# Kernel tuning notes

Measured on AMD Instinct MI355X. Metric: run time of the kernel, lower is better.

Reference implementation:

```python
import jax, jax.numpy as jnp
import numpy as np

THETA = 10000.0
B, S, D, H = 2, 2048, 1024, 16
DK = D // H


def setup_inputs() -> dict:
    key = jax.random.key(0)
    k1, k2, k3 = jax.random.split(key, 3)
    x = jax.random.normal(k1, (B, S, D), jnp.float32)
    # trunc_normal init approximated by scaled normal (std = 2/(d_k+d_model))
    weight = jax.random.normal(k2, (3, H, DK, D), jnp.float32) * (2.0 / (DK + D))
    wo_weight = jax.random.normal(k3, (D, H * DK), jnp.float32) * (2.0 / (2 * D))
    token_positions = jnp.arange(S, dtype=jnp.int32)
    return {"x": x, "token_positions": token_positions, "weight": weight, "wo_weight": wo_weight}


def _rope(x, cos, sin):
    # x: (..., seq, d_k); rotate interleaved pairs
    x1 = jnp.stack((-x[..., 1::2], x[..., ::2]), axis=-1).reshape(x.shape)
    return x * cos + x1 * sin


def _masked_softmax(scores, mask):
    # matches reference: exp(x - rowmax over ALL entries), zero masked, normalize, zero again
    e = jnp.exp(scores - jnp.max(scores, axis=-1, keepdims=True))
    e = jnp.where(mask, e, 0.0)
    a = e / jnp.sum(e, axis=-1, keepdims=True)
    return jnp.where(mask, a, 0.0)


def reference(x, token_positions, weight, wo_weight):
    dk = weight.shape[2]
    seq_len = x.shape[-2]
    # fused QKV projection: (b, 3, h, s, dk)
    qkv = jnp.einsum('bsd,qhkd->bqhsk', x, weight)
    # RoPE tables from token positions
    pos = token_positions.astype(jnp.float32)[:, None]          # (s, 1)
    kidx = jnp.arange(1, dk // 2 + 1, dtype=jnp.float32)[None]  # (1, dk/2)
    theta = pos / (THETA ** ((2.0 * kidx - 2.0) / dk))          # (s, dk/2)
    cos = jnp.repeat(jnp.cos(theta), 2, axis=-1)                # (s, dk)
    sin = jnp.repeat(jnp.sin(theta), 2, axis=-1)
    q = _rope(qkv[:, 0], cos, sin)   # (b, h, s, dk)
    k = _rope(qkv[:, 1], cos, sin)
    v = qkv[:, 2]
    scores = jnp.einsum('bhqd,bhkd->bhqk', q, k) / jnp.sqrt(jnp.float32(dk))
    mask = jnp.tril(jnp.ones((seq_len, seq_len), dtype=bool))
    att = _masked_softmax(scores, mask)
    out = jnp.einsum('bhqk,bhkd->bhqd', att, v)                 # (b, h, s, dv)
    out = jnp.transpose(out, (0, 2, 1, 3)).reshape(*x.shape[:-1], -1)  # (b, s, h*dv)
    return jnp.einsum('bsi,oi->bso', out, wo_weight)
```

## Files before the change

kernel.cpp:

```cpp
#include <hip/hip_runtime.h>
#include <hip/hip_bf16.h>
#include <math.h>

#define B_   2
#define S_   2048
#define D_   1024
#define H_   16
#define DK_  64
#define NQKV 3072
#define M_   (B_ * S_)

typedef unsigned short u16;
typedef unsigned int   u32;
typedef __attribute__((ext_vector_type(8))) short short8;
typedef __attribute__((ext_vector_type(4))) float f32x4;
typedef __attribute__((ext_vector_type(4))) u16   u16x4;

typedef const __attribute__((address_space(1))) void* gvptr;
typedef __attribute__((address_space(3))) void* lvptr;

#define QSCALE 0.18033688011f

#if __has_builtin(__builtin_amdgcn_exp2f)
#define EXP2F(x) __builtin_amdgcn_exp2f(x)
#else
#define EXP2F(x) __expf(0.69314718056f * (x))
#endif

__device__ __forceinline__ u16 f2bf(float f) {
  union { float f; u32 u; } v; v.f = f;
  u32 r = v.u + 0x7FFF + ((v.u >> 16) & 1);
  return (u16)(r >> 16);
}
__device__ __forceinline__ float bf2f(u16 h) {
  union { u32 u; float f; } v; v.u = ((u32)h) << 16;
  return v.f;
}
__device__ __forceinline__ u32 cvtpk_bf16(float lo, float hi) {
  u32 r;
  asm("v_cvt_pk_bf16_f32 %0, %1, %2" : "=v"(r) : "v"(lo), "v"(hi));
  return r;
}

#define MEMFENCE() asm volatile("" ::: "memory")
#define RAW_BARRIER() do { MEMFENCE(); __builtin_amdgcn_s_barrier(); MEMFENCE(); } while (0)

#define SWZ(r) ((((r) & 7) ^ ((((r) >> 3) & 1) << 2)))

__global__ void rope_cs_kernel(const int* __restrict__ pos,
                               float2* __restrict__ cs) {
  int idx = blockIdx.x * 256 + threadIdx.x;
  int i = idx & 31;
  int s = idx >> 5;
  double p = (double)pos[s];
  double t = p * pow(10000.0, -(double)i / 32.0);
  cs[idx] = make_float2((float)cos(t), (float)sin(t));
}

#define N4X (M_ * D_ / 4)
#define N4W (NQKV * D_ / 4)
#define N4WO (D_ * D_ / 4)
__global__ void cvt_all_kernel(const float* __restrict__ x,
                               const float* __restrict__ w,
                               const float* __restrict__ wo,
                               u16* __restrict__ dst) {
  int i = blockIdx.x * 256 + threadIdx.x;
  float4 v;
  if (i < N4X)            v = ((const float4*)x)[i];
  else if (i < N4X + N4W) v = ((const float4*)w)[i - N4X];
  else                    v = ((const float4*)wo)[i - (N4X + N4W)];
  u16x4 o;
  o[0] = f2bf(v.x); o[1] = f2bf(v.y); o[2] = f2bf(v.z); o[3] = f2bf(v.w);
  ((u16x4*)dst)[i] = o;
}

template<bool OUT_BF16, bool ROPE>
__global__ __launch_bounds__(256) void gemm_nt_mfma(const u16* __restrict__ A,
                                                    const u16* __restrict__ Bm,
                                                    void* __restrict__ Cout,
                                                    const float2* __restrict__ cstab,
                                                    int Nd, int Kd) {
  __shared__ u16 As[128 * 64];
  __shared__ u16 Bs[128 * 64];
  const int t  = threadIdx.x;
  const int w  = t >> 6, l = t & 63;
  const int g  = l >> 4, ln = l & 15;
  const int wm = w >> 1, wn = w & 1;
  const int m0 = blockIdx.y * 128, n0 = blockIdx.x * 128;

  const f32x4 vzero = {0.f, 0.f, 0.f, 0.f};
  f32x4 acc[4][4];
#pragma unroll
  for (int i = 0; i < 4; ++i)
#pragma unroll
    for (int j = 0; j < 4; ++j) acc[i][j] = vzero;

  for (int k0 = 0; k0 < Kd; k0 += 64) {
    __syncthreads();
#pragma unroll
    for (int p = 0; p < 4; ++p) {
      int c = p * 256 + t;
      int r = c >> 3, sx = (c & 7) ^ (r & 7);
      __builtin_amdgcn_global_load_lds(
          (gvptr)(A + (size_t)(m0 + r) * Kd + k0 + sx * 8),
          (lvptr)(&As[(p * 256 + w * 64) * 8]), 16, 0, 0);
      __builtin_amdgcn_global_load_lds(
          (gvptr)(Bm + (size_t)(n0 + r) * Kd + k0 + sx * 8),
          (lvptr)(&Bs[(p * 256 + w * 64) * 8]), 16, 0, 0);
    }
    __syncthreads();

#pragma unroll
    for (int ks = 0; ks < 2; ++ks) {
      short8 af[4], bf[4];
#pragma unroll
      for (int i = 0; i < 4; ++i) {
        int ra = wm * 64 + i * 16 + ln;
        af[i] = *(const short8*)&As[ra * 64 + (((ks * 4 + g) ^ (ra & 7)) * 8)];
        int rb = wn * 64 + i * 16 + ln;
        bf[i] = *(const short8*)&Bs[rb * 64 + (((ks * 4 + g) ^ (rb & 7)) * 8)];
      }
#pragma unroll
      for (int i = 0; i < 4; ++i)
#pragma unroll
        for (int j = 0; j < 4; ++j)
          acc[i][j] = __builtin_amdgcn_mfma_f32_16x16x32_bf16(af[i], bf[j], acc[i][j], 0, 0, 0);
    }
  }

  if (ROPE && n0 < 2048) {
#pragma unroll
    for (int i = 0; i < 4; ++i)
#pragma unroll
      for (int r = 0; r < 4; ++r) {
        int rowi = m0 + wm * 64 + i * 16 + g * 4 + r;
        int srow = rowi & (S_ - 1);
#pragma unroll
        for (int j = 0; j < 4; ++j) {
          int dk = j * 16 + ln;
          float2 cs = cstab[srow * 32 + (dk >> 1)];
          float v = acc[i][j][r];
          float p = __shfl_xor(v, 1);
          float sn = (ln & 1) ? cs.y : -cs.y;
          float rot = fmaf(p, sn, v * cs.x);
          ((u16*)Cout)[(size_t)rowi * Nd + n0 + wn * 64 + j * 16 + ln] = f2bf(rot);
        }
      }
  } else {
#pragma unroll
    for (int i = 0; i < 4; ++i)
#pragma unroll
      for (int j = 0; j < 4; ++j)
#pragma unroll
        for (int r = 0; r < 4; ++r) {
          size_t row = (size_t)(m0 + wm * 64 + i * 16 + g * 4 + r);
          size_t col = (size_t)(n0 + wn * 64 + j * 16 + ln);
          if (OUT_BF16) ((u16*)Cout)[row * Nd + col] = f2bf(acc[i][j][r]);
          else          ((float*)Cout)[row * Nd + col] = acc[i][j][r];
        }
  }
}

__global__ __launch_bounds__(256) void v_transpose_kernel(const u16* __restrict__ qkvb,
                                                          u16* __restrict__ Vt) {
  __shared__ u16 tile[64][72];
  const int t = threadIdx.x;
  const int s0 = blockIdx.x * 64, h = blockIdx.y, b = blockIdx.z;
  {
    int r = t >> 2, cs = (t & 3) * 16;
    const u16* src = qkvb + (size_t)(b * S_ + s0 + r) * NQKV + 2048 + h * 64 + cs;
    u16 v[16];
    *(uint4*)&v[0] = *(const uint4*)src;
    *(uint4*)&v[8] = *(const uint4*)(src + 8);
#pragma unroll
    for (int j = 0; j < 16; ++j) tile[cs + j][r] = v[j];
  }
  __syncthreads();
  {
    int d = t >> 2, ss = (t & 3) * 16;
    u16 o[16];
#pragma unroll
    for (int j = 0; j < 16; ++j) o[j] = tile[d][ss + j];
    u16* dst = Vt + ((size_t)(b * H_ + h) * 64 + d) * S_ + s0 + ss;
    *(uint4*)&dst[0] = *(uint4*)&o[0];
    *(uint4*)&dst[8] = *(uint4*)&o[8];
  }
}

__global__ __launch_bounds__(512) void attn_mfma(const u16* __restrict__ qkvb,
                                                 const u16* __restrict__ Vt,
                                                 u16* __restrict__ attb) {
  __shared__ u16 Ks[3][64 * 64];
  __shared__ u16 Vs[3][64 * 64];
  const int t = threadIdx.x;
  const int w = t >> 6, l = t & 63;
  const int g = l >> 4, ln = l & 15;
  const int h = blockIdx.y, b = blockIdx.z;
  const size_t bS = (size_t)b * S_;
  const u16* Kbase = qkvb + bS * NQKV + D_ + h * 64;
  const u16* Vbase = Vt + (size_t)(b * H_ + h) * 64 * S_;

  const int sr = t >> 3;
  const int ssx = (t & 7) ^ SWZ(sr);
  auto stage = [&](int buf, int k0) {
    __builtin_amdgcn_global_load_lds(
        (gvptr)(Kbase + (size_t)(k0 + sr) * NQKV + ssx * 8),
        (lvptr)(&Ks[buf][w * 512]), 16, 0, 0);
    __builtin_amdgcn_global_load_lds(
        (gvptr)(Vbase + (size_t)sr * S_ + k0 + ssx * 8),
        (lvptr)(&Vs[buf][w * 512]), 16, 0, 0);
  };

  const f32x4 vzero = {0.f, 0.f, 0.f, 0.f};

#pragma unroll 1
  for (int half = 0; half < 2; ++half) {
    const int tq = (half == 0) ? (15 - blockIdx.x) : blockIdx.x;
    const int q0 = tq * 128;
    const int nt = 2 * tq + 2;
    const int qg = q0 + w * 16 + ln;
    const int wqmax = q0 + w * 16 + 15;

    short8 qf[2];
    {
      const u16* qrow = qkvb + (bS + q0 + w * 16 + ln) * NQKV + h * 64;
      qf[0] = *(const short8*)(qrow + g * 8);
      qf[1] = *(const short8*)(qrow + 32 + g * 8);
#pragma unroll
      for (int kx = 0; kx < 2; ++kx)
#pragma unroll
        for (int e = 0; e < 8; ++e)
          qf[kx][e] = (short)f2bf(bf2f((u16)qf[kx][e]) * QSCALE);
    }

    f32x4 o[4];
#pragma unroll
    for (int dt = 0; dt < 4; ++dt) o[dt] = vzero;
    float mrun = -INFINITY, lrun = 0.f;

    stage(0, 0);
    stage(1, 64);
    int cur = 0;

#pragma unroll 1
    for (int kt = 0; kt < nt; ++kt) {
      const int k0 = kt * 64;
      if (kt + 2 < nt) {
        int pre = cur + 2; if (pre >= 3) pre -= 3;
        stage(pre, k0 + 128);
        asm volatile("s_waitcnt vmcnt(4)" ::: "memory");
      } else if (kt + 1 < nt) {
        asm volatile("s_waitcnt vmcnt(2)" ::: "memory");
      } else {
        asm volatile("s_waitcnt vmcnt(0)" ::: "memory");
      }
      RAW_BARRIER();

      if (k0 <= wqmax) {
        f32x4 sacc[4];
#pragma unroll
        for (int st = 0; st < 4; ++st) sacc[st] = vzero;
        __builtin_amdgcn_s_setprio(1);
#pragma unroll
        for (int st = 0; st < 4; ++st) {
          const int pr = ((ln >> 2) << 3) + ((st & 1) << 2) + (ln & 3) + ((st >> 1) << 5);
#pragma unroll
          for (int ks = 0; ks < 2; ++ks) {
            short8 kf = *(const short8*)&Ks[cur][pr * 64 + (((ks * 4 + g) ^ SWZ(pr)) * 8)];
            sacc[st] = __builtin_amdgcn_mfma_f32_16x16x32_bf16(kf, qf[ks], sacc[st], 0, 0, 0);
          }
        }
        __builtin_amdgcn_s_setprio(0);

        float tmax = -INFINITY;
        if (k0 + 63 > q0 + w * 16) {
#pragma unroll
          for (int st = 0; st < 4; ++st)
#pragma unroll
            for (int r = 0; r < 4; ++r) {
              int key = k0 + g * 8 + ((st & 1) << 2) + r + ((st >> 1) << 5);
              if (key > qg) sacc[st][r] = -INFINITY;
              tmax = fmaxf(tmax, sacc[st][r]);
            }
        } else {
#pragma unroll
          for (int st = 0; st < 4; ++st)
#pragma unroll
            for (int r = 0; r < 4; ++r) tmax = fmaxf(tmax, sacc[st][r]);
        }
        tmax = fmaxf(tmax, __shfl_xor(tmax, 16));
        tmax = fmaxf(tmax, __shfl_xor(tmax, 32));
        float al = 1.f, mnew = mrun;
        if (!__all(tmax <= mrun + 8.0f)) {
          mnew = fmaxf(mrun, tmax);
          al = EXP2F(mrun - mnew);
#pragma unroll
          for (int r = 0; r < 4; ++r) {
            float srs = __shfl(al, g * 4 + r);
#pragma unroll
            for (int dt = 0; dt < 4; ++dt) o[dt][r] *= srs;
          }
        }
        float lsum = 0.f;
#pragma unroll
        for (int st = 0; st < 4; ++st)
#pragma unroll
          for (int r = 0; r < 4; ++r) {
            float pe = EXP2F(sacc[st][r] - mnew);
            sacc[st][r] = pe;
            lsum += pe;
          }
        lsum += __shfl_xor(lsum, 16);
        lsum += __shfl_xor(lsum, 32);
        lrun = lrun * al + lsum;
        mrun = mnew;

        union { u32 u[4]; short8 v; } pa[2];
        pa[0].u[0] = cvtpk_bf16(sacc[0][0], sacc[0][1]);
        pa[0].u[1] = cvtpk_bf16(sacc[0][2], sacc[0][3]);
        pa[0].u[2] = cvtpk_bf16(sacc[1][0], sacc[1][1]);
        pa[0].u[3] = cvtpk_bf16(sacc[1][2], sacc[1][3]);
        pa[1].u[0] = cvtpk_bf16(sacc[2][0], sacc[2][1]);
        pa[1].u[1] = cvtpk_bf16(sacc[2][2], sacc[2][3]);
        pa[1].u[2] = cvtpk_bf16(sacc[3][0], sacc[3][1]);
        pa[1].u[3] = cvtpk_bf16(sacc[3][2], sacc[3][3]);

        __builtin_amdgcn_s_setprio(1);
#pragma unroll
        for (int ks = 0; ks < 2; ++ks)
#pragma unroll
          for (int dt = 0; dt < 4; ++dt) {
            const int dr = dt * 16 + ln;
            short8 vf = *(const short8*)&Vs[cur][dr * 64 + (((ks * 4 + g) ^ SWZ(dr)) * 8)];
            o[dt] = __builtin_amdgcn_mfma_f32_16x16x32_bf16(pa[ks].v, vf, o[dt], 0, 0, 0);
          }
        __builtin_amdgcn_s_setprio(0);
      }

      asm volatile("s_waitcnt lgkmcnt(0)" ::: "memory");
      RAW_BARRIER();
      cur = (cur == 2) ? 0 : cur + 1;
    }

    float linv = 1.f / lrun;
#pragma unroll
    for (int r = 0; r < 4; ++r) {
      float ir = __shfl(linv, g * 4 + r);
      size_t row = bS + q0 + w * 16 + g * 4 + r;
#pragma unroll
      for (int dt = 0; dt < 4; ++dt)
        attb[row * D_ + h * 64 + dt * 16 + ln] = f2bf(o[dt][r] * ir);
    }
    asm volatile("s_waitcnt vmcnt(0)" ::: "memory");
  }
}

extern "C" void kernel_launch(void* const* d_in, const int* in_sizes, int n_in,
                              void* d_out, int out_size, void* d_ws, size_t ws_size,
                              hipStream_t stream) {
  (void)in_sizes; (void)n_in; (void)out_size; (void)ws_size;
  const float* x   = (const float*)d_in[0];
  const int*   pos = (const int*)d_in[1];
  const float* w   = (const float*)d_in[2];
  const float* wo  = (const float*)d_in[3];
  float* out = (float*)d_out;

  u16* qkvb = (u16*)d_ws;
  u16* Vt   = qkvb + (size_t)M_ * NQKV;
  u16* attb = Vt + (size_t)B_ * H_ * 64 * S_;
  u16* xb   = attb + (size_t)M_ * D_;
  u16* wb   = xb + (size_t)M_ * D_;
  u16* wob  = wb + (size_t)NQKV * D_;
  float2* cstab = (float2*)(wob + (size_t)D_ * D_);

  rope_cs_kernel<<<(S_ * 32) / 256, 256, 0, stream>>>(pos, cstab);

  cvt_all_kernel<<<(N4X + N4W + N4WO) / 256, 256, 0, stream>>>(x, w, wo, xb);

  gemm_nt_mfma<true, true><<<dim3(NQKV / 128, M_ / 128), 256, 0, stream>>>(
      xb, wb, qkvb, cstab, NQKV, D_);

  v_transpose_kernel<<<dim3(S_ / 64, H_, B_), 256, 0, stream>>>(qkvb, Vt);

  attn_mfma<<<dim3(8, H_, B_), 512, 0, stream>>>(qkvb, Vt, attb);

  gemm_nt_mfma<false, false><<<dim3(D_ / 128, M_ / 128), 256, 0, stream>>>(
      attb, wob, out, nullptr, D_, D_);
}
```

Baseline: 208.1 us.

## Double-buffer LDS tiles in GEMM to overlap global loads with MFMA

The GEMM kernel now keeps two LDS buffers for the A and B tiles. It issues the global-to-LDS loads for the next K tile before computing the current one, using explicit vmcnt waits and raw barriers in place of two __syncthreads per iteration. It also raises wave priority around the MFMA section. The aim is to hide global load latency behind matrix math, at the cost of doubling LDS use (64KB per block), which may reduce occupancy.

```diff
diff --git a/kernel.cpp b/kernel.cpp
--- a/kernel.cpp
+++ b/kernel.cpp
@@ -80,14 +80,29 @@
                                                     void* __restrict__ Cout,
                                                     const float2* __restrict__ cstab,
                                                     int Nd, int Kd) {
-  __shared__ u16 As[128 * 64];
-  __shared__ u16 Bs[128 * 64];
+  __shared__ u16 As[2][128 * 64];
+  __shared__ u16 Bs[2][128 * 64];
   const int t  = threadIdx.x;
   const int w  = t >> 6, l = t & 63;
   const int g  = l >> 4, ln = l & 15;
   const int wm = w >> 1, wn = w & 1;
   const int m0 = blockIdx.y * 128, n0 = blockIdx.x * 128;
 
+  const int sr = t >> 3;
+  auto stage = [&](int buf, int k0) {
+#pragma unroll
+    for (int p = 0; p < 4; ++p) {
+      int r = p * 32 + sr;
+      int sx = (t & 7) ^ (r & 7);
+      __builtin_amdgcn_global_load_lds(
+          (gvptr)(A + (size_t)(m0 + r) * Kd + k0 + sx * 8),
+          (lvptr)(&As[buf][(p * 256 + w * 64) * 8]), 16, 0, 0);
+      __builtin_amdgcn_global_load_lds(
+          (gvptr)(Bm + (size_t)(n0 + r) * Kd + k0 + sx * 8),
+          (lvptr)(&Bs[buf][(p * 256 + w * 64) * 8]), 16, 0, 0);
+    }
+  };
+
   const f32x4 vzero = {0.f, 0.f, 0.f, 0.f};
   f32x4 acc[4][4];
 #pragma unroll
@@ -95,30 +110,29 @@
 #pragma unroll
     for (int j = 0; j < 4; ++j) acc[i][j] = vzero;
 
-  for (int k0 = 0; k0 < Kd; k0 += 64) {
-    __syncthreads();
-#pragma unroll
-    for (int p = 0; p < 4; ++p) {
-      int c = p * 256 + t;
-      int r = c >> 3, sx = (c & 7) ^ (r & 7);
-      __builtin_amdgcn_global_load_lds(
-          (gvptr)(A + (size_t)(m0 + r) * Kd + k0 + sx * 8),
-          (lvptr)(&As[(p * 256 + w * 64) * 8]), 16, 0, 0);
-      __builtin_amdgcn_global_load_lds(
-          (gvptr)(Bm + (size_t)(n0 + r) * Kd + k0 + sx * 8),
-          (lvptr)(&Bs[(p * 256 + w * 64) * 8]), 16, 0, 0);
-    }
-    __syncthreads();
-
+  const int nkt = Kd >> 6;
+  stage(0, 0);
+  int cur = 0;
+#pragma unroll 1
+  for (int kt = 0; kt < nkt; ++kt) {
+    if (kt + 1 < nkt) {
+      stage(cur ^ 1, (kt + 1) * 64);
+      asm volatile("s_waitcnt vmcnt(8)" ::: "memory");
+    } else {
+      asm volatile("s_waitcnt vmcnt(0)" ::: "memory");
+    }
+    RAW_BARRIER();
+
+    __builtin_amdgcn_s_setprio(1);
 #pragma unroll
     for (int ks = 0; ks < 2; ++ks) {
       short8 af[4], bf[4];
 #pragma unroll
       for (int i = 0; i < 4; ++i) {
         int ra = wm * 64 + i * 16 + ln;
-        af[i] = *(const short8*)&As[ra * 64 + (((ks * 4 + g) ^ (ra & 7)) * 8)];
+        af[i] = *(const short8*)&As[cur][ra * 64 + (((ks * 4 + g) ^ (ra & 7)) * 8)];
         int rb = wn * 64 + i * 16 + ln;
-        bf[i] = *(const short8*)&Bs[rb * 64 + (((ks * 4 + g) ^ (rb & 7)) * 8)];
+        bf[i] = *(const short8*)&Bs[cur][rb * 64 + (((ks * 4 + g) ^ (rb & 7)) * 8)];
       }
 #pragma unroll
       for (int i = 0; i < 4; ++i)
@@ -126,6 +140,11 @@
         for (int j = 0; j < 4; ++j)
           acc[i][j] = __builtin_amdgcn_mfma_f32_16x16x32_bf16(af[i], bf[j], acc[i][j], 0, 0, 0);
     }
+    __builtin_amdgcn_s_setprio(0);
+
+    asm volatile("s_waitcnt lgkmcnt(0)" ::: "memory");
+    RAW_BARRIER();
+    cur ^= 1;
   }
 
   if (ROPE && n0 < 2048) {
```

After: 203.2 us. 1.02x faster.
